# Performance work log

Hardware: AMD Instinct MI355X
Metric: run time of the kernel (lower is better)

## Reference

```python
import jax, jax.numpy as jnp
import numpy as np

DIM = 1024
HEADS = 16
HEAD_DIM = DIM // HEADS
HIDDEN = int(DIM * 4.0)
B, N = 8, 1024


def setup_inputs() -> dict:
    key = jax.random.key(0)
    ks = jax.random.split(key, 12)
    s = lambda fan_in: 1.0 / np.sqrt(fan_in)
    return {
        "x": jax.random.normal(ks[0], (B, N, DIM), jnp.float32),
        "ln_g": jnp.ones((DIM,), jnp.float32),
        "ln_b": jnp.zeros((DIM,), jnp.float32),
        "w_qkv": jax.random.normal(ks[1], (DIM, 3 * DIM), jnp.float32) * s(DIM),
        "b_qkv": jnp.zeros((3 * DIM,), jnp.float32),
        "w_proj": jax.random.normal(ks[2], (DIM, DIM), jnp.float32) * s(DIM),
        "b_proj": jnp.zeros((DIM,), jnp.float32),
        "w_fc1": jax.random.normal(ks[3], (DIM, HIDDEN), jnp.float32) * s(DIM),
        "b_fc1": jnp.zeros((HIDDEN,), jnp.float32),
        "w_fc2": jax.random.normal(ks[4], (HIDDEN, DIM), jnp.float32) * s(HIDDEN),
        "b_fc2": jnp.zeros((DIM,), jnp.float32),
    }


def _layernorm(x, g, b, eps=1e-6):
    mu = jnp.mean(x, axis=-1, keepdims=True)
    var = jnp.var(x, axis=-1, keepdims=True)
    return (x - mu) * jax.lax.rsqrt(var + eps) * g + b


def _attention(x, w_qkv, b_qkv, w_proj, b_proj):
    b, n, d = x.shape
    qkv = x @ w_qkv + b_qkv                       # [B,N,3D]
    qkv = qkv.reshape(b, n, 3, HEADS, HEAD_DIM)
    qkv = jnp.transpose(qkv, (2, 0, 3, 1, 4))     # [3,B,H,N,hd]
    q, k, v = qkv[0], qkv[1], qkv[2]
    scale = HEAD_DIM ** -0.5
    scores = jnp.einsum('bhqd,bhkd->bhqk', q, k) * scale
    attn = jax.nn.softmax(scores, axis=-1)
    out = jnp.einsum('bhqk,bhkd->bhqd', attn, v)  # [B,H,N,hd]
    out = jnp.transpose(out, (0, 2, 1, 3)).reshape(b, n, d)
    return out @ w_proj + b_proj


def reference(x, ln_g, ln_b, w_qkv, b_qkv, w_proj, b_proj, w_fc1, b_fc1, w_fc2, b_fc2):
    # NOTE: original module reuses the same LayerNorm params for both norms.
    h = x + _attention(_layernorm(x, ln_g, ln_b), w_qkv, b_qkv, w_proj, b_proj)
    y = _layernorm(h, ln_g, ln_b)
    y = jax.nn.gelu(y @ w_fc1 + b_fc1, approximate=False)  # exact GELU (torch default)
    y = y @ w_fc2 + b_fc2
    return h + y
```

## Files before the change

### kernel.cpp

```cpp
#include <hip/hip_runtime.h>
#include <math.h>

typedef unsigned short ushort_t;
typedef __attribute__((ext_vector_type(8))) short bf16x8;
typedef __attribute__((ext_vector_type(4))) float f32x4;

#define TOKENS 8192
#define DIMD   1024
#define TDIM   3072
#define HIDN   4096
#define NHEADS 16
#define HD     64

__device__ inline float bf2f(ushort_t h){ return __uint_as_float(((unsigned)h)<<16); }
__device__ inline ushort_t f2bf(float f){
  unsigned u = __float_as_uint(f);
  unsigned r = (u + 0x7fffu + ((u>>16)&1u)) >> 16;
  return (ushort_t)r;
}
__device__ inline float gelu_f(float x){
  float u = 1.5957691216f * x * fmaf(0.044715f, x*x, 1.0f);
  return x / (1.0f + __expf(-u));
}

__device__ inline void glds16(const ushort_t* g, ushort_t* l){
  __builtin_amdgcn_global_load_lds(
      (const __attribute__((address_space(1))) void*)g,
      (__attribute__((address_space(3))) void*)l,
      16, 0, 0);
}

__global__ __launch_bounds__(256)
void convT_f32_bf16(const float* __restrict__ in, ushort_t* __restrict__ out,
                    int R, int C)
{
  __shared__ ushort_t t[64*65];
  const int c0 = blockIdx.x*64, r0 = blockIdx.y*64;
  for (int idx = threadIdx.x; idx < 4096; idx += 256) {
    int r = idx>>6, c = idx&63;
    t[r*65+c] = f2bf(in[(size_t)(r0+r)*C + c0+c]);
  }
  __syncthreads();
  for (int idx = threadIdx.x; idx < 4096; idx += 256) {
    int c = idx>>6, r = idx&63;
    out[(size_t)(c0+c)*R + r0+r] = t[r*65+c];
  }
}

__global__ __launch_bounds__(256)
void ln_kernel(const float* __restrict__ xin, const float* __restrict__ g,
               const float* __restrict__ bta, ushort_t* __restrict__ out)
{
  const int tid = threadIdx.x;
  const size_t base = (size_t)blockIdx.x * DIMD;
  float v[4];
  #pragma unroll
  for (int i=0;i<4;i++) v[i] = xin[base + tid + i*256];
  float s  = v[0]+v[1]+v[2]+v[3];
  float s2 = v[0]*v[0]+v[1]*v[1]+v[2]*v[2]+v[3]*v[3];
  #pragma unroll
  for (int off=32; off; off>>=1){ s += __shfl_xor(s, off); s2 += __shfl_xor(s2, off); }
  __shared__ float rs[4], rs2[4];
  const int wave = tid>>6, lane = tid&63;
  if (lane==0){ rs[wave]=s; rs2[wave]=s2; }
  __syncthreads();
  s  = rs[0]+rs[1]+rs[2]+rs[3];
  s2 = rs2[0]+rs2[1]+rs2[2]+rs2[3];
  const float mean = s * (1.f/DIMD);
  const float var  = s2 * (1.f/DIMD) - mean*mean;
  const float rstd = rsqrtf(var + 1e-6f);
  #pragma unroll
  for (int i=0;i<4;i++){
    int c = tid + i*256;
    out[base+c] = f2bf((v[i]-mean)*rstd*g[c] + bta[c]);
  }
}

template<int RES, int OUTF, int ACT, int QKVW>
__global__ __launch_bounds__(256)
void gemm128(const ushort_t* __restrict__ A, const ushort_t* __restrict__ Bt,
             const float* __restrict__ bias, const float* __restrict__ res,
             void* __restrict__ out, int M, int N, int K)
{
  __shared__ ushort_t As[128*32];
  __shared__ ushort_t Bs[128*32];
  const int tid = threadIdx.x, wave = tid>>6, lane = tid&63;
  const int bm = blockIdx.y, bn = blockIdx.x;

  const int sr  = lane>>2;
  const int scw = ((lane&3) ^ (sr&3))*8;
  const ushort_t* Ag0 = A  + (size_t)(bm*128 + wave*32 + sr)*K + scw;
  const ushort_t* Ag1 = Ag0 + (size_t)16*K;
  const ushort_t* Bg0 = Bt + (size_t)(bn*128 + wave*32 + sr)*K + scw;
  const ushort_t* Bg1 = Bg0 + (size_t)16*K;
  ushort_t* Asw0 = &As[(wave*32)*32];
  ushort_t* Asw1 = &As[(wave*32+16)*32];
  ushort_t* Bsw0 = &Bs[(wave*32)*32];
  ushort_t* Bsw1 = &Bs[(wave*32+16)*32];

  f32x4 acc[4][4];
  #pragma unroll
  for (int m=0;m<4;m++)
    #pragma unroll
    for (int n=0;n<4;n++) acc[m][n] = (f32x4){0.f,0.f,0.f,0.f};

  const int row = lane&15, quad = lane>>4;
  const int mrow = (wave&1)*64, ncol = (wave>>1)*64;
  const int chsw = (quad ^ (row&3))*8;

  for (int k0=0; k0<K; k0+=32){
    __syncthreads();
    glds16(Ag0+k0, Asw0); glds16(Ag1+k0, Asw1);
    glds16(Bg0+k0, Bsw0); glds16(Bg1+k0, Bsw1);
    __syncthreads();
    bf16x8 af[4], bfr[4];
    #pragma unroll
    for (int m=0;m<4;m++) af[m]  = *(const bf16x8*)&As[(mrow+m*16+row)*32 + chsw];
    #pragma unroll
    for (int n=0;n<4;n++) bfr[n] = *(const bf16x8*)&Bs[(ncol+n*16+row)*32 + chsw];
    #pragma unroll
    for (int m=0;m<4;m++)
      #pragma unroll
      for (int n=0;n<4;n++)
        acc[m][n] = __builtin_amdgcn_mfma_f32_16x16x32_bf16(af[m], bfr[n], acc[m][n], 0,0,0);
  }

  const int r0 = bm*128 + mrow + quad*4;
  #pragma unroll
  for (int n=0;n<4;n++){
    const int gc = bn*128 + ncol + n*16 + row;
    const float bv = bias[gc];
    #pragma unroll
    for (int m=0;m<4;m++){
      #pragma unroll
      for (int r=0;r<4;r++){
        const int grow = r0 + m*16 + r;
        float v = acc[m][n][r] + bv;
        if (ACT) v = gelu_f(v);
        if (QKVW) {
          const int which = gc>>10, hh = (gc>>6)&15, d = gc&63;
          const int bb = grow>>10, nn = grow&1023;
          ((ushort_t*)out)[((size_t)(which*128 + bb*16 + hh)<<16) + nn*64 + d] = f2bf(v);
        } else {
          const size_t idx = (size_t)grow*N + gc;
          if (RES)  v += res[idx];
          if (OUTF) ((float*)out)[idx] = v;
          else      ((ushort_t*)out)[idx] = f2bf(v);
        }
      }
    }
  }
}

#define AST 72
__global__ __launch_bounds__(256)
void attn_mfma(const ushort_t* __restrict__ qkv3, ushort_t* __restrict__ out)
{
  __shared__ ushort_t Ks[2][64*64];
  __shared__ ushort_t Vt[2][64*AST];
  __shared__ ushort_t Ps[4][16*AST];

  const int tid = threadIdx.x, wave = tid>>6, lane = tid&63;
  const int row = lane&15, quad = lane>>4;
  const int qt = blockIdx.x & 15;
  const int bh = blockIdx.x >> 4;
  const ushort_t* qp = qkv3 + ((size_t)bh<<16);
  const ushort_t* kp = qkv3 + ((size_t)(128+bh)<<16);
  const ushort_t* vp = qkv3 + ((size_t)(256+bh)<<16);

  const ushort_t* qrp = qp + (size_t)(qt*64 + wave*16 + row)*64 + quad*8;
  bf16x8 qa0 = *(const bf16x8*)(qrp);
  bf16x8 qa1 = *(const bf16x8*)(qrp + 32);

  const int krow = (lane>>3);
  const int kch  = ((lane&7) ^ krow)*8;

  f32x4 acc_o[4];
  #pragma unroll
  for (int nt=0;nt<4;nt++) acc_o[nt] = (f32x4){0.f,0.f,0.f,0.f};
  float lp[4] = {0.f,0.f,0.f,0.f};
  uint4 va[2];

  #pragma unroll
  for (int i=0;i<2;i++)
    glds16(kp + (size_t)(wave*16 + i*8 + krow)*64 + kch, &Ks[0][(wave*16+i*8)*64]);
  #pragma unroll
  for (int i=0;i<2;i++){
    int idx=i*256+tid, ch=idx>>6, key=idx&63;
    va[i] = *(const uint4*)(vp + (size_t)key*64 + ch*8);
  }
  #pragma unroll
  for (int i=0;i<2;i++){
    int idx=i*256+tid, ch=idx>>6, key=idx&63;
    ushort_t tmp[8]; *(uint4*)tmp = va[i];
    #pragma unroll
    for (int j=0;j<8;j++) Vt[0][(ch*8+j)*AST + key] = tmp[j];
  }

  for (int jt=0; jt<16; ++jt){
    const int p = jt&1;
    __syncthreads();
    if (jt<15){
      #pragma unroll
      for (int i=0;i<2;i++)
        glds16(kp + (size_t)((jt+1)*64 + wave*16 + i*8 + krow)*64 + kch,
               &Ks[1-p][(wave*16+i*8)*64]);
      #pragma unroll
      for (int i=0;i<2;i++){
        int idx=i*256+tid, ch=idx>>6, key=idx&63;
        va[i] = *(const uint4*)(vp + (size_t)((jt+1)*64+key)*64 + ch*8);
      }
    }

    #pragma unroll
    for (int ct=0;ct<4;ct++){
      const int key = ct*16 + row;
      f32x4 s = (f32x4){0.f,0.f,0.f,0.f};
      bf16x8 b0 = *(const bf16x8*)&Ks[p][key*64 + ((quad   ^(row&7))*8)];
      bf16x8 b1 = *(const bf16x8*)&Ks[p][key*64 + (((quad+4)^(row&7))*8)];
      s = __builtin_amdgcn_mfma_f32_16x16x32_bf16(qa0, b0, s, 0,0,0);
      s = __builtin_amdgcn_mfma_f32_16x16x32_bf16(qa1, b1, s, 0,0,0);
      #pragma unroll
      for (int r=0;r<4;r++){
        float pr = __expf(fmaf(s[r], 0.125f, -3.0f));
        lp[r] += pr;
        Ps[wave][(quad*4+r)*AST + ct*16 + row] = f2bf(pr);
      }
    }

    bf16x8 pa0 = *(const bf16x8*)&Ps[wave][row*AST + quad*8];
    bf16x8 pa1 = *(const bf16x8*)&Ps[wave][row*AST + 32 + quad*8];
    #pragma unroll
    for (int nt=0;nt<4;nt++){
      bf16x8 vb0 = *(const bf16x8*)&Vt[p][(nt*16+row)*AST + quad*8];
      bf16x8 vb1 = *(const bf16x8*)&Vt[p][(nt*16+row)*AST + 32 + quad*8];
      acc_o[nt] = __builtin_amdgcn_mfma_f32_16x16x32_bf16(pa0, vb0, acc_o[nt], 0,0,0);
      acc_o[nt] = __builtin_amdgcn_mfma_f32_16x16x32_bf16(pa1, vb1, acc_o[nt], 0,0,0);
    }

    if (jt<15){
      #pragma unroll
      for (int i=0;i<2;i++){
        int idx=i*256+tid, ch=idx>>6, key=idx&63;
        ushort_t tmp[8]; *(uint4*)tmp = va[i];
        #pragma unroll
        for (int j=0;j<8;j++) Vt[1-p][(ch*8+j)*AST + key] = tmp[j];
      }
    }
  }

  #pragma unroll
  for (int r=0;r<4;r++){
    float l = lp[r];
    l += __shfl_xor(l,1); l += __shfl_xor(l,2);
    l += __shfl_xor(l,4); l += __shfl_xor(l,8);
    lp[r] = l;
  }
  const int b = bh>>4, h = bh&15;
  #pragma unroll
  for (int nt=0;nt<4;nt++){
    #pragma unroll
    for (int r=0;r<4;r++){
      size_t o = (size_t)(b*1024 + qt*64 + wave*16 + quad*4 + r)*DIMD
               + h*64 + nt*16 + row;
      out[o] = f2bf(acc_o[nt][r] / lp[r]);
    }
  }
}

extern "C" void kernel_launch(void* const* d_in, const int* in_sizes, int n_in,
                              void* d_out, int out_size, void* d_ws, size_t ws_size,
                              hipStream_t stream)
{
  const float* x      = (const float*)d_in[0];
  const float* ln_g   = (const float*)d_in[1];
  const float* ln_b   = (const float*)d_in[2];
  const float* w_qkv  = (const float*)d_in[3];
  const float* b_qkv  = (const float*)d_in[4];
  const float* w_proj = (const float*)d_in[5];
  const float* b_proj = (const float*)d_in[6];
  const float* w_fc1  = (const float*)d_in[7];
  const float* b_fc1  = (const float*)d_in[8];
  const float* w_fc2  = (const float*)d_in[9];
  const float* b_fc2  = (const float*)d_in[10];

  char* ws = (char*)d_ws;
  ushort_t* wqkvT  = (ushort_t*)(ws + 0);
  ushort_t* wprojT = (ushort_t*)(ws + 6291456);
  ushort_t* wfc1T  = (ushort_t*)(ws + 8388608);
  ushort_t* wfc2T  = (ushort_t*)(ws + 16777216);
  ushort_t* lnbuf  = (ushort_t*)(ws + 25165824);
  ushort_t* qkv3   = (ushort_t*)(ws + 41943040);
  float*    hbuf   = (float*)   (ws + 41943040);
  ushort_t* gbuf   = (ushort_t*)(ws + 75497472);

  convT_f32_bf16<<<dim3(TDIM/64, DIMD/64), 256, 0, stream>>>(w_qkv,  wqkvT,  DIMD, TDIM);
  convT_f32_bf16<<<dim3(DIMD/64, DIMD/64), 256, 0, stream>>>(w_proj, wprojT, DIMD, DIMD);
  convT_f32_bf16<<<dim3(HIDN/64, DIMD/64), 256, 0, stream>>>(w_fc1,  wfc1T,  DIMD, HIDN);
  convT_f32_bf16<<<dim3(DIMD/64, HIDN/64), 256, 0, stream>>>(w_fc2,  wfc2T,  HIDN, DIMD);

  ln_kernel<<<TOKENS, 256, 0, stream>>>(x, ln_g, ln_b, lnbuf);
  gemm128<0,0,0,1><<<dim3(TDIM/128, TOKENS/128), 256, 0, stream>>>(
      lnbuf, wqkvT, b_qkv, nullptr, qkv3, TOKENS, TDIM, DIMD);
  attn_mfma<<<128*16, 256, 0, stream>>>(qkv3, lnbuf);
  gemm128<1,1,0,0><<<dim3(DIMD/128, TOKENS/128), 256, 0, stream>>>(
      lnbuf, wprojT, b_proj, x, hbuf, TOKENS, DIMD, DIMD);
  ln_kernel<<<TOKENS, 256, 0, stream>>>(hbuf, ln_g, ln_b, lnbuf);
  gemm128<0,0,1,0><<<dim3(HIDN/128, TOKENS/128), 256, 0, stream>>>(
      lnbuf, wfc1T, b_fc1, nullptr, gbuf, TOKENS, HIDN, DIMD);
  gemm128<1,1,0,0><<<dim3(DIMD/128, TOKENS/128), 256, 0, stream>>>(
      gbuf, wfc2T, b_fc2, hbuf, d_out, TOKENS, DIMD, HIDN);
}
```

Before: 569.3 us.

## Merge weight transposes with first LayerNorm and use 64x128 tiles for N=1024 GEMMs

Folds the four weight-transpose launches and the first LayerNorm into one prep kernel that dispatches on block index, cutting launch count and letting the independent work overlap. Adds a 64x128-tile GEMM variant for the proj and fc2 GEMMs, whose output is only 1024 wide, doubling their block count from 512 to 1024 so more of the GPU's compute units are busy. The smaller tiles reuse each loaded tile less and issue more loads per FLOP.

Result: no change. 579.1 us (+1.7%).

```diff
diff --git a/kernel.cpp b/kernel.cpp
--- a/kernel.cpp
+++ b/kernel.cpp
@@ -30,12 +30,12 @@
       16, 0, 0);
 }
 
-__global__ __launch_bounds__(256)
-void convT_f32_bf16(const float* __restrict__ in, ushort_t* __restrict__ out,
-                    int R, int C)
-{
-  __shared__ ushort_t t[64*65];
-  const int c0 = blockIdx.x*64, r0 = blockIdx.y*64;
+__device__ inline void transpose_tile(const float* __restrict__ in,
+                                      ushort_t* __restrict__ out,
+                                      int R, int C, int cx, int ry,
+                                      ushort_t* t )
+{
+  const int c0 = cx*64, r0 = ry*64;
   for (int idx = threadIdx.x; idx < 4096; idx += 256) {
     int r = idx>>6, c = idx&63;
     t[r*65+c] = f2bf(in[(size_t)(r0+r)*C + c0+c]);
@@ -47,33 +47,65 @@
   }
 }
 
+__device__ inline void ln_row(const float* __restrict__ xin, int rowid,
+                              const float* __restrict__ g,
+                              const float* __restrict__ bta,
+                              ushort_t* __restrict__ out,
+                              float* rs )
+{
+  const int tid = threadIdx.x;
+  const size_t base = (size_t)rowid * DIMD;
+  float v[4];
+  #pragma unroll
+  for (int i=0;i<4;i++) v[i] = xin[base + tid + i*256];
+  float s  = v[0]+v[1]+v[2]+v[3];
+  float s2 = v[0]*v[0]+v[1]*v[1]+v[2]*v[2]+v[3]*v[3];
+  #pragma unroll
+  for (int off=32; off; off>>=1){ s += __shfl_xor(s, off); s2 += __shfl_xor(s2, off); }
+  const int wave = tid>>6, lane = tid&63;
+  if (lane==0){ rs[wave]=s; rs[4+wave]=s2; }
+  __syncthreads();
+  s  = rs[0]+rs[1]+rs[2]+rs[3];
+  s2 = rs[4]+rs[5]+rs[6]+rs[7];
+  const float mean = s * (1.f/DIMD);
+  const float var  = s2 * (1.f/DIMD) - mean*mean;
+  const float rstd = rsqrtf(var + 1e-6f);
+  #pragma unroll
+  for (int i=0;i<4;i++){
+    int c = tid + i*256;
+    out[base+c] = f2bf((v[i]-mean)*rstd*g[c] + bta[c]);
+  }
+}
+
+__global__ __launch_bounds__(256)
+void prep_kernel(const float* __restrict__ x,
+                 const float* __restrict__ ln_g, const float* __restrict__ ln_b,
+                 ushort_t* __restrict__ lnbuf,
+                 const float* __restrict__ w_qkv,  ushort_t* __restrict__ wqkvT,
+                 const float* __restrict__ w_proj, ushort_t* __restrict__ wprojT,
+                 const float* __restrict__ w_fc1,  ushort_t* __restrict__ wfc1T,
+                 const float* __restrict__ w_fc2,  ushort_t* __restrict__ wfc2T)
+{
+  __shared__ char smem[64*65*2];
+  const int bid = blockIdx.x;
+  if (bid < TOKENS) {
+    ln_row(x, bid, ln_g, ln_b, lnbuf, (float*)smem);
+    return;
+  }
+  int t = bid - TOKENS;
+  ushort_t* ts = (ushort_t*)smem;
+  if (t < 768)        transpose_tile(w_qkv,  wqkvT,  DIMD, TDIM, t%48, t/48, ts);
+  else if (t < 1024){ t -= 768;  transpose_tile(w_proj, wprojT, DIMD, DIMD, t%16, t/16, ts); }
+  else if (t < 2048){ t -= 1024; transpose_tile(w_fc1,  wfc1T,  DIMD, HIDN, t%64, t/64, ts); }
+  else              { t -= 2048; transpose_tile(w_fc2,  wfc2T,  HIDN, DIMD, t%16, t/16, ts); }
+}
+
 __global__ __launch_bounds__(256)
 void ln_kernel(const float* __restrict__ xin, const float* __restrict__ g,
                const float* __restrict__ bta, ushort_t* __restrict__ out)
 {
-  const int tid = threadIdx.x;
-  const size_t base = (size_t)blockIdx.x * DIMD;
-  float v[4];
-  #pragma unroll
-  for (int i=0;i<4;i++) v[i] = xin[base + tid + i*256];
-  float s  = v[0]+v[1]+v[2]+v[3];
-  float s2 = v[0]*v[0]+v[1]*v[1]+v[2]*v[2]+v[3]*v[3];
-  #pragma unroll
-  for (int off=32; off; off>>=1){ s += __shfl_xor(s, off); s2 += __shfl_xor(s2, off); }
-  __shared__ float rs[4], rs2[4];
-  const int wave = tid>>6, lane = tid&63;
-  if (lane==0){ rs[wave]=s; rs2[wave]=s2; }
-  __syncthreads();
-  s  = rs[0]+rs[1]+rs[2]+rs[3];
-  s2 = rs2[0]+rs2[1]+rs2[2]+rs2[3];
-  const float mean = s * (1.f/DIMD);
-  const float var  = s2 * (1.f/DIMD) - mean*mean;
-  const float rstd = rsqrtf(var + 1e-6f);
-  #pragma unroll
-  for (int i=0;i<4;i++){
-    int c = tid + i*256;
-    out[base+c] = f2bf((v[i]-mean)*rstd*g[c] + bta[c]);
-  }
+  __shared__ float rs[8];
+  ln_row(xin, blockIdx.x, g, bta, out, rs);
 }
 
 template<int RES, int OUTF, int ACT, int QKVW>
@@ -152,6 +184,74 @@
   }
 }
 
+template<int RES, int OUTF, int ACT>
+__global__ __launch_bounds__(256)
+void gemm64x128(const ushort_t* __restrict__ A, const ushort_t* __restrict__ Bt,
+                const float* __restrict__ bias, const float* __restrict__ res,
+                void* __restrict__ out, int M, int N, int K)
+{
+  __shared__ ushort_t As[64*32];
+  __shared__ ushort_t Bs[128*32];
+  const int tid = threadIdx.x, wave = tid>>6, lane = tid&63;
+  const int bm = blockIdx.y, bn = blockIdx.x;
+
+  const int sr  = lane>>2;
+  const int scw = ((lane&3) ^ (sr&3))*8;
+  const ushort_t* Ag0 = A  + (size_t)(bm*64  + wave*16 + sr)*K + scw;
+  const ushort_t* Bg0 = Bt + (size_t)(bn*128 + wave*32 + sr)*K + scw;
+  const ushort_t* Bg1 = Bg0 + (size_t)16*K;
+  ushort_t* Asw0 = &As[(wave*16)*32];
+  ushort_t* Bsw0 = &Bs[(wave*32)*32];
+  ushort_t* Bsw1 = &Bs[(wave*32+16)*32];
+
+  f32x4 acc[2][4];
+  #pragma unroll
+  for (int m=0;m<2;m++)
+    #pragma unroll
+    for (int n=0;n<4;n++) acc[m][n] = (f32x4){0.f,0.f,0.f,0.f};
+
+  const int row = lane&15, quad = lane>>4;
+  const int mrow = (wave&1)*32, ncol = (wave>>1)*64;
+  const int chsw = (quad ^ (row&3))*8;
+
+  for (int k0=0; k0<K; k0+=32){
+    __syncthreads();
+    glds16(Ag0+k0, Asw0);
+    glds16(Bg0+k0, Bsw0); glds16(Bg1+k0, Bsw1);
+    __syncthreads();
+    bf16x8 af[2], bfr[4];
+    #pragma unroll
+    for (int m=0;m<2;m++) af[m]  = *(const bf16x8*)&As[(mrow+m*16+row)*32 + chsw];
+    #pragma unroll
+    for (int n=0;n<4;n++) bfr[n] = *(const bf16x8*)&Bs[(ncol+n*16+row)*32 + chsw];
+    #pragma unroll
+    for (int m=0;m<2;m++)
+      #pragma unroll
+      for (int n=0;n<4;n++)
+        acc[m][n] = __builtin_amdgcn_mfma_f32_16x16x32_bf16(af[m], bfr[n], acc[m][n], 0,0,0);
+  }
+
+  const int r0 = bm*64 + mrow + quad*4;
+  #pragma unroll
+  for (int n=0;n<4;n++){
+    const int gc = bn*128 + ncol + n*16 + row;
+    const float bv = bias[gc];
+    #pragma unroll
+    for (int m=0;m<2;m++){
+      #pragma unroll
+      for (int r=0;r<4;r++){
+        const int grow = r0 + m*16 + r;
+        float v = acc[m][n][r] + bv;
+        if (ACT) v = gelu_f(v);
+        const size_t idx = (size_t)grow*N + gc;
+        if (RES)  v += res[idx];
+        if (OUTF) ((float*)out)[idx] = v;
+        else      ((ushort_t*)out)[idx] = f2bf(v);
+      }
+    }
+  }
+}
+
 #define AST 72
 __global__ __launch_bounds__(256)
 void attn_mfma(const ushort_t* __restrict__ qkv3, ushort_t* __restrict__ out)
@@ -294,20 +394,18 @@
   float*    hbuf   = (float*)   (ws + 41943040);
   ushort_t* gbuf   = (ushort_t*)(ws + 75497472);
 
-  convT_f32_bf16<<<dim3(TDIM/64, DIMD/64), 256, 0, stream>>>(w_qkv,  wqkvT,  DIMD, TDIM);
-  convT_f32_bf16<<<dim3(DIMD/64, DIMD/64), 256, 0, stream>>>(w_proj, wprojT, DIMD, DIMD);
-  convT_f32_bf16<<<dim3(HIDN/64, DIMD/64), 256, 0, stream>>>(w_fc1,  wfc1T,  DIMD, HIDN);
-  convT_f32_bf16<<<dim3(DIMD/64, HIDN/64), 256, 0, stream>>>(w_fc2,  wfc2T,  HIDN, DIMD);
-
-  ln_kernel<<<TOKENS, 256, 0, stream>>>(x, ln_g, ln_b, lnbuf);
+  prep_kernel<<<TOKENS + 3072, 256, 0, stream>>>(
+      x, ln_g, ln_b, lnbuf,
+      w_qkv, wqkvT, w_proj, wprojT, w_fc1, wfc1T, w_fc2, wfc2T);
+
   gemm128<0,0,0,1><<<dim3(TDIM/128, TOKENS/128), 256, 0, stream>>>(
       lnbuf, wqkvT, b_qkv, nullptr, qkv3, TOKENS, TDIM, DIMD);
   attn_mfma<<<128*16, 256, 0, stream>>>(qkv3, lnbuf);
-  gemm128<1,1,0,0><<<dim3(DIMD/128, TOKENS/128), 256, 0, stream>>>(
+  gemm64x128<1,1,0><<<dim3(DIMD/128, TOKENS/64), 256, 0, stream>>>(
       lnbuf, wprojT, b_proj, x, hbuf, TOKENS, DIMD, DIMD);
   ln_kernel<<<TOKENS, 256, 0, stream>>>(hbuf, ln_g, ln_b, lnbuf);
   gemm128<0,0,1,0><<<dim3(HIDN/128, TOKENS/128), 256, 0, stream>>>(
       lnbuf, wfc1T, b_fc1, nullptr, gbuf, TOKENS, HIDN, DIMD);
-  gemm128<1,1,0,0><<<dim3(DIMD/128, TOKENS/128), 256, 0, stream>>>(
+  gemm64x128<1,1,0><<<dim3(DIMD/128, TOKENS/64), 256, 0, stream>>>(
       gbuf, wfc2T, b_fc2, hbuf, d_out, TOKENS, DIMD, HIDN);
 }
```

## Double-buffer GEMM LDS tiles and merge weight-transpose and first LayerNorm launches

Applied to the files above, without the earlier changes.

The GEMM kernel now keeps two LDS buffers for A and B and prefetches the next K tile while running MFMAs on the current one. This drops one barrier per K step and aims to hide global-to-LDS load latency. The four weight-transpose kernels and the first LayerNorm are also merged into one prep kernel, which cuts launch overhead and lets the tiles run concurrently. Risks: doubled LDS use per block may lower occupancy. Correctness of the prefetch also depends on the compiler placing wait counts correctly for the async global_load_lds before the next barrier, and a conservative wait could erase the overlap.

Result: faster. 537.6 us (-5.6%).

```diff
diff --git a/kernel.cpp b/kernel.cpp
--- a/kernel.cpp
+++ b/kernel.cpp
@@ -30,12 +30,12 @@
       16, 0, 0);
 }
 
-__global__ __launch_bounds__(256)
-void convT_f32_bf16(const float* __restrict__ in, ushort_t* __restrict__ out,
-                    int R, int C)
-{
-  __shared__ ushort_t t[64*65];
-  const int c0 = blockIdx.x*64, r0 = blockIdx.y*64;
+__device__ inline void transpose_tile(const float* __restrict__ in,
+                                      ushort_t* __restrict__ out,
+                                      int R, int C, int cx, int ry,
+                                      ushort_t* t )
+{
+  const int c0 = cx*64, r0 = ry*64;
   for (int idx = threadIdx.x; idx < 4096; idx += 256) {
     int r = idx>>6, c = idx&63;
     t[r*65+c] = f2bf(in[(size_t)(r0+r)*C + c0+c]);
@@ -47,33 +47,65 @@
   }
 }
 
+__device__ inline void ln_row(const float* __restrict__ xin, int rowid,
+                              const float* __restrict__ g,
+                              const float* __restrict__ bta,
+                              ushort_t* __restrict__ out,
+                              float* rs )
+{
+  const int tid = threadIdx.x;
+  const size_t base = (size_t)rowid * DIMD;
+  float v[4];
+  #pragma unroll
+  for (int i=0;i<4;i++) v[i] = xin[base + tid + i*256];
+  float s  = v[0]+v[1]+v[2]+v[3];
+  float s2 = v[0]*v[0]+v[1]*v[1]+v[2]*v[2]+v[3]*v[3];
+  #pragma unroll
+  for (int off=32; off; off>>=1){ s += __shfl_xor(s, off); s2 += __shfl_xor(s2, off); }
+  const int wave = tid>>6, lane = tid&63;
+  if (lane==0){ rs[wave]=s; rs[4+wave]=s2; }
+  __syncthreads();
+  s  = rs[0]+rs[1]+rs[2]+rs[3];
+  s2 = rs[4]+rs[5]+rs[6]+rs[7];
+  const float mean = s * (1.f/DIMD);
+  const float var  = s2 * (1.f/DIMD) - mean*mean;
+  const float rstd = rsqrtf(var + 1e-6f);
+  #pragma unroll
+  for (int i=0;i<4;i++){
+    int c = tid + i*256;
+    out[base+c] = f2bf((v[i]-mean)*rstd*g[c] + bta[c]);
+  }
+}
+
+__global__ __launch_bounds__(256)
+void prep_kernel(const float* __restrict__ x,
+                 const float* __restrict__ ln_g, const float* __restrict__ ln_b,
+                 ushort_t* __restrict__ lnbuf,
+                 const float* __restrict__ w_qkv,  ushort_t* __restrict__ wqkvT,
+                 const float* __restrict__ w_proj, ushort_t* __restrict__ wprojT,
+                 const float* __restrict__ w_fc1,  ushort_t* __restrict__ wfc1T,
+                 const float* __restrict__ w_fc2,  ushort_t* __restrict__ wfc2T)
+{
+  __shared__ char smem[64*65*2];
+  const int bid = blockIdx.x;
+  if (bid < TOKENS) {
+    ln_row(x, bid, ln_g, ln_b, lnbuf, (float*)smem);
+    return;
+  }
+  int t = bid - TOKENS;
+  ushort_t* ts = (ushort_t*)smem;
+  if (t < 768)        transpose_tile(w_qkv,  wqkvT,  DIMD, TDIM, t%48, t/48, ts);
+  else if (t < 1024){ t -= 768;  transpose_tile(w_proj, wprojT, DIMD, DIMD, t%16, t/16, ts); }
+  else if (t < 2048){ t -= 1024; transpose_tile(w_fc1,  wfc1T,  DIMD, HIDN, t%64, t/64, ts); }
+  else              { t -= 2048; transpose_tile(w_fc2,  wfc2T,  HIDN, DIMD, t%16, t/16, ts); }
+}
+
 __global__ __launch_bounds__(256)
 void ln_kernel(const float* __restrict__ xin, const float* __restrict__ g,
                const float* __restrict__ bta, ushort_t* __restrict__ out)
 {
-  const int tid = threadIdx.x;
-  const size_t base = (size_t)blockIdx.x * DIMD;
-  float v[4];
-  #pragma unroll
-  for (int i=0;i<4;i++) v[i] = xin[base + tid + i*256];
-  float s  = v[0]+v[1]+v[2]+v[3];
-  float s2 = v[0]*v[0]+v[1]*v[1]+v[2]*v[2]+v[3]*v[3];
-  #pragma unroll
-  for (int off=32; off; off>>=1){ s += __shfl_xor(s, off); s2 += __shfl_xor(s2, off); }
-  __shared__ float rs[4], rs2[4];
-  const int wave = tid>>6, lane = tid&63;
-  if (lane==0){ rs[wave]=s; rs2[wave]=s2; }
-  __syncthreads();
-  s  = rs[0]+rs[1]+rs[2]+rs[3];
-  s2 = rs2[0]+rs2[1]+rs2[2]+rs2[3];
-  const float mean = s * (1.f/DIMD);
-  const float var  = s2 * (1.f/DIMD) - mean*mean;
-  const float rstd = rsqrtf(var + 1e-6f);
-  #pragma unroll
-  for (int i=0;i<4;i++){
-    int c = tid + i*256;
-    out[base+c] = f2bf((v[i]-mean)*rstd*g[c] + bta[c]);
-  }
+  __shared__ float rs[8];
+  ln_row(xin, blockIdx.x, g, bta, out, rs);
 }
 
 template<int RES, int OUTF, int ACT, int QKVW>
@@ -82,8 +114,8 @@
              const float* __restrict__ bias, const float* __restrict__ res,
              void* __restrict__ out, int M, int N, int K)
 {
-  __shared__ ushort_t As[128*32];
-  __shared__ ushort_t Bs[128*32];
+  __shared__ ushort_t As[2][128*32];
+  __shared__ ushort_t Bs[2][128*32];
   const int tid = threadIdx.x, wave = tid>>6, lane = tid&63;
   const int bm = blockIdx.y, bn = blockIdx.x;
 
@@ -93,10 +125,10 @@
   const ushort_t* Ag1 = Ag0 + (size_t)16*K;
   const ushort_t* Bg0 = Bt + (size_t)(bn*128 + wave*32 + sr)*K + scw;
   const ushort_t* Bg1 = Bg0 + (size_t)16*K;
-  ushort_t* Asw0 = &As[(wave*32)*32];
-  ushort_t* Asw1 = &As[(wave*32+16)*32];
-  ushort_t* Bsw0 = &Bs[(wave*32)*32];
-  ushort_t* Bsw1 = &Bs[(wave*32+16)*32];
+  const int aw0 = (wave*32)*32, aw1 = (wave*32+16)*32;
+
+  glds16(Ag0, &As[0][aw0]); glds16(Ag1, &As[0][aw1]);
+  glds16(Bg0, &Bs[0][aw0]); glds16(Bg1, &Bs[0][aw1]);
 
   f32x4 acc[4][4];
   #pragma unroll
@@ -108,16 +140,20 @@
   const int mrow = (wave&1)*64, ncol = (wave>>1)*64;
   const int chsw = (quad ^ (row&3))*8;
 
-  for (int k0=0; k0<K; k0+=32){
+  const int NK = K>>5;
+  for (int kt=0; kt<NK; ++kt){
+    const int p = kt&1;
     __syncthreads();
-    glds16(Ag0+k0, Asw0); glds16(Ag1+k0, Asw1);
-    glds16(Bg0+k0, Bsw0); glds16(Bg1+k0, Bsw1);
-    __syncthreads();
+    if (kt+1 < NK){
+      const int k1 = (kt+1)<<5;
+      glds16(Ag0+k1, &As[1-p][aw0]); glds16(Ag1+k1, &As[1-p][aw1]);
+      glds16(Bg0+k1, &Bs[1-p][aw0]); glds16(Bg1+k1, &Bs[1-p][aw1]);
+    }
     bf16x8 af[4], bfr[4];
     #pragma unroll
-    for (int m=0;m<4;m++) af[m]  = *(const bf16x8*)&As[(mrow+m*16+row)*32 + chsw];
-    #pragma unroll
-    for (int n=0;n<4;n++) bfr[n] = *(const bf16x8*)&Bs[(ncol+n*16+row)*32 + chsw];
+    for (int m=0;m<4;m++) af[m]  = *(const bf16x8*)&As[p][(mrow+m*16+row)*32 + chsw];
+    #pragma unroll
+    for (int n=0;n<4;n++) bfr[n] = *(const bf16x8*)&Bs[p][(ncol+n*16+row)*32 + chsw];
     #pragma unroll
     for (int m=0;m<4;m++)
       #pragma unroll
@@ -294,12 +330,10 @@
   float*    hbuf   = (float*)   (ws + 41943040);
   ushort_t* gbuf   = (ushort_t*)(ws + 75497472);
 
-  convT_f32_bf16<<<dim3(TDIM/64, DIMD/64), 256, 0, stream>>>(w_qkv,  wqkvT,  DIMD, TDIM);
-  convT_f32_bf16<<<dim3(DIMD/64, DIMD/64), 256, 0, stream>>>(w_proj, wprojT, DIMD, DIMD);
-  convT_f32_bf16<<<dim3(HIDN/64, DIMD/64), 256, 0, stream>>>(w_fc1,  wfc1T,  DIMD, HIDN);
-  convT_f32_bf16<<<dim3(DIMD/64, HIDN/64), 256, 0, stream>>>(w_fc2,  wfc2T,  HIDN, DIMD);
-
-  ln_kernel<<<TOKENS, 256, 0, stream>>>(x, ln_g, ln_b, lnbuf);
+  prep_kernel<<<TOKENS + 3072, 256, 0, stream>>>(
+      x, ln_g, ln_b, lnbuf,
+      w_qkv, wqkvT, w_proj, wprojT, w_fc1, wfc1T, w_fc2, wfc2T);
+
   gemm128<0,0,0,1><<<dim3(TDIM/128, TOKENS/128), 256, 0, stream>>>(
       lnbuf, wqkvT, b_qkv, nullptr, qkv3, TOKENS, TDIM, DIMD);
   attn_mfma<<<128*16, 256, 0, stream>>>(qkv3, lnbuf);
```
